# Optimization experiments

Hardware: AMD Instinct MI355X
Metric: run time of the kernel (lower is better)

Reference implementation:

```python
import jax, jax.numpy as jnp
import numpy as np

H_IMG, W_IMG = 16, 64
HK, WK = 7, 11
DIM, NUM_HEADS = 384, 8
BATCH = 32
SEQ = H_IMG * W_IMG  # 1024


def build_local_mask():
    # Faithful to the torch constructor: for each query position (i,j), a
    # (hk x wk) window of zeros in a padded canvas; everything else -inf.
    h, w, hk, wk = H_IMG, W_IMG, HK, WK
    mask = np.ones((h * w, h + hk - 1, w + wk - 1), dtype=np.float32)
    for i in range(h):
        for j in range(w):
            mask[w * i + j, i:i + hk, j:j + wk] = 0.0
    mask_c = mask[:, hk // 2:h + hk // 2, wk // 2:w + wk // 2].reshape(h * w, h * w)
    out = np.where(mask_c == 1.0, np.float32(-np.inf), mask_c).astype(np.float32)
    return jnp.asarray(out)  # [S, S]


def setup_inputs() -> dict:
    key = jax.random.key(0)
    k1, k2, k3, k4 = jax.random.split(key, 4)
    s = 1.0 / np.sqrt(DIM)
    return {
        "x": jax.random.normal(k1, (BATCH, SEQ, DIM), dtype=jnp.float32),
        "w_qkv": jax.random.normal(k2, (DIM, 3 * DIM), dtype=jnp.float32) * s,
        "w_proj": jax.random.normal(k3, (DIM, DIM), dtype=jnp.float32) * s,
        "b_proj": jax.random.normal(k4, (DIM,), dtype=jnp.float32) * 0.01,
        "mask": build_local_mask(),
    }


def reference(x, w_qkv, w_proj, b_proj, mask):
    B, S, C = x.shape
    H = NUM_HEADS
    D = C // H
    scale = D ** -0.5
    qkv = (x @ w_qkv).reshape(B, S, 3, H, D)
    qkv = jnp.transpose(qkv, (2, 0, 3, 1, 4))  # [3, B, H, S, D]
    q, k, v = qkv[0] * scale, qkv[1], qkv[2]
    attn = jnp.einsum("bhsd,bhtd->bhst", q, k)  # [B, H, S, S]
    attn = attn + mask[None, None]               # additive local-window bias
    attn = jax.nn.softmax(attn, axis=-1)
    out = jnp.einsum("bhst,bhtd->bhsd", attn, v)
    out = jnp.transpose(out, (0, 2, 1, 3)).reshape(B, S, C)
    return out @ w_proj + b_proj
```

## Files before the change

kernel.cpp:

```cpp
#include <hip/hip_runtime.h>
#include <hip/hip_bf16.h>


typedef __attribute__((ext_vector_type(8))) unsigned short ushort8;
typedef __attribute__((ext_vector_type(8))) short short8v;
typedef __attribute__((ext_vector_type(4))) float floatx4;

__device__ __forceinline__ float bf2f(unsigned short u) {
  union { unsigned int i; float f; } x;
  x.i = ((unsigned int)u) << 16;
  return x.f;
}

__device__ __forceinline__ unsigned short f2bu(float f) {
  union { float f; unsigned int i; } x;
  x.f = f;
  unsigned int lsb = (x.i >> 16) & 1u;
  x.i += 0x7FFFu + lsb;
  return (unsigned short)(x.i >> 16);
}

__device__ __forceinline__ unsigned int cvtpk_bf16(float lo, float hi) {
  unsigned int r;
  asm("v_cvt_pk_bf16_f32 %0, %1, %2" : "=v"(r) : "v"(lo), "v"(hi));
  return r;
}

__device__ __forceinline__ void gload_lds16(const void* g, void* l) {
  __builtin_amdgcn_global_load_lds(
      (const __attribute__((address_space(1))) unsigned int*)g,
      (__attribute__((address_space(3))) unsigned int*)l, 16, 0, 0);
}

__global__ __launch_bounds__(256) void transpose_cvt(
    const float* __restrict__ in, unsigned short* __restrict__ out, int R, int C) {
  __shared__ float t[32][33];
  const int c0 = blockIdx.x * 32, r0 = blockIdx.y * 32;
  const int tx = threadIdx.x, ty = threadIdx.y;
  #pragma unroll
  for (int rr = ty; rr < 32; rr += 8) t[rr][tx] = in[(size_t)(r0 + rr) * C + c0 + tx];
  __syncthreads();
  #pragma unroll
  for (int rr = ty; rr < 32; rr += 8)
    out[(size_t)(c0 + rr) * R + r0 + tx] = f2bu(t[tx][rr]);
}

__global__ __launch_bounds__(512) void gemm_qkv(
    const float* __restrict__ X,
    const unsigned short* __restrict__ Bt,
    unsigned short* __restrict__ qws, unsigned short* __restrict__ kws,
    unsigned short* __restrict__ vtws)
{
  __shared__ unsigned short smem[32768];
  const int tid = threadIdx.x;
  const int lane = tid & 63, w = tid >> 6;
  const int wm = w & 3, wn = w >> 2;

  const int nbx = gridDim.x;
  const int nwg = nbx * gridDim.y;
  const int bid = blockIdx.y * nbx + blockIdx.x;
  const int swz = (bid & 7) * (nwg >> 3) + (bid >> 3);
  const int n0 = (swz % nbx) * 128;
  const int m0 = (swz / nbx) * 128;

  floatx4 acc[2][4];
  #pragma unroll
  for (int mi = 0; mi < 2; ++mi)
    #pragma unroll
    for (int ni = 0; ni < 4; ++ni)
      acc[mi][ni] = (floatx4){0.f, 0.f, 0.f, 0.f};

  const int arow = tid >> 2;
  const int aslot = tid & 3;
  const int adst = arow * 64 + ((aslot * 16) ^ ((arow & 3) << 4));
  const float* asrc = X + (size_t)(m0 + arow) * 384 + aslot * 8;

  auto ASB = [&](int buf) -> char* { return (char*)smem + buf * 8192; };
  auto BSB = [&](int buf) -> char* { return (char*)smem + 32768 + buf * 8192; };

  float4 bank0[4], bank1[4];

  auto LOADA = [&](float4* bank, int p) {
    #pragma unroll
    for (int tile = 0; tile < 2; ++tile) {
      const float* s = asrc + (p * 2 + tile) * 32;
      bank[tile * 2 + 0] = *reinterpret_cast<const float4*>(s);
      bank[tile * 2 + 1] = *reinterpret_cast<const float4*>(s + 4);
    }
  };
  auto DSWRITE = [&](const float4* bank, int p) {
    #pragma unroll
    for (int tile = 0; tile < 2; ++tile) {
      const float4 f0 = bank[tile * 2 + 0];
      const float4 f1 = bank[tile * 2 + 1];
      uint4 v;
      v.x = cvtpk_bf16(f0.x, f0.y); v.y = cvtpk_bf16(f0.z, f0.w);
      v.z = cvtpk_bf16(f1.x, f1.y); v.w = cvtpk_bf16(f1.z, f1.w);
      *reinterpret_cast<uint4*>(ASB(2 * (p & 1) + tile) + adst) = v;
    }
  };
  const int srow = tid >> 2;
  const int kslot16 = (tid & 3) * 16;
  auto BGLOAD = [&](int p) {
    #pragma unroll
    for (int tile = 0; tile < 2; ++tile) {
      const int t = p * 2 + tile;
      const int kb = kslot16 ^ ((srow & 3) << 4);
      gload_lds16((const char*)Bt + (size_t)(n0 + srow) * 768 + t * 64 + kb,
                  BSB(2 * (p & 1) + tile) + w * 1024);
    }
  };
  auto COMPUTE = [&](int buf) {
    short8v a[2], b[4];
    const int kgb = (lane >> 4) * 16;
    #pragma unroll
    for (int mi = 0; mi < 2; ++mi) {
      const int r = wm * 32 + mi * 16 + (lane & 15);
      a[mi] = *reinterpret_cast<const short8v*>(
          ASB(buf) + r * 64 + (kgb ^ ((r & 3) << 4)));
    }
    #pragma unroll
    for (int ni = 0; ni < 4; ++ni) {
      const int r = wn * 64 + ni * 16 + (lane & 15);
      b[ni] = *reinterpret_cast<const short8v*>(
          BSB(buf) + r * 64 + (kgb ^ ((r & 3) << 4)));
    }
    #pragma unroll
    for (int mi = 0; mi < 2; ++mi)
      #pragma unroll
      for (int ni = 0; ni < 4; ++ni)
        acc[mi][ni] = __builtin_amdgcn_mfma_f32_16x16x32_bf16(
            a[mi], b[ni], acc[mi][ni], 0, 0, 0);
  };

  LOADA(bank0, 0);
  BGLOAD(0);
  LOADA(bank1, 1);
  BGLOAD(1);
  asm volatile("s_waitcnt vmcnt(8)" ::: "memory");
  DSWRITE(bank0, 0);
  asm volatile("s_waitcnt vmcnt(2)" ::: "memory");
  DSWRITE(bank1, 1);
  LOADA(bank0, 2);
  asm volatile("s_waitcnt lgkmcnt(0)" ::: "memory");
  __builtin_amdgcn_s_barrier();

  #pragma unroll
  for (int s = 0; s < 6; ++s) {
    __builtin_amdgcn_s_setprio(1);
    COMPUTE(2 * (s & 1));
    COMPUTE(2 * (s & 1) + 1);
    __builtin_amdgcn_s_setprio(0);
    asm volatile("s_waitcnt lgkmcnt(0)" ::: "memory");
    if (s + 2 <= 5) {
      asm volatile("s_waitcnt vmcnt(4)" ::: "memory");
    } else if (s + 1 <= 5) {
      asm volatile("s_waitcnt vmcnt(0)" ::: "memory");
    }
    __builtin_amdgcn_s_barrier();
    if (s + 2 <= 5) {
      BGLOAD(s + 2);
      asm volatile("s_waitcnt vmcnt(2)" ::: "memory");
      DSWRITE((s & 1) ? bank1 : bank0, s + 2);
      if (s + 3 <= 5) LOADA((s & 1) ? bank0 : bank1, s + 3);
    }
  }

  const int col_l = lane & 15;
  const int row_l = (lane >> 4) * 4;
  const float QSCALE = 0.14433756729740643f;
  const int which = n0 / 384;

  if (which < 2) {
    unsigned short* dstb = (which == 0) ? qws : kws;
    const float scale = (which == 0) ? QSCALE : 1.f;
    #pragma unroll
    for (int ni = 0; ni < 4; ++ni) {
      const int cg = n0 + wn * 64 + ni * 16 + col_l;
      const int rem = cg - which * 384;
      const int h = rem / 48;
      const int d = rem - h * 48;
      #pragma unroll
      for (int mi = 0; mi < 2; ++mi) {
        #pragma unroll
        for (int reg = 0; reg < 4; ++reg) {
          const int r = m0 + wm * 32 + mi * 16 + row_l + reg;
          const int bb = r >> 10, s = r & 1023;
          dstb[(((size_t)(bb * 8 + h)) * 1024 + s) * 48 + d] =
              f2bu(acc[mi][ni][reg] * scale);
        }
      }
    }
  } else {
    unsigned short* T = smem;
    #pragma unroll
    for (int ni = 0; ni < 4; ++ni) {
      const int col = wn * 64 + ni * 16 + col_l;
      #pragma unroll
      for (int mi = 0; mi < 2; ++mi) {
        const int rowb = wm * 32 + mi * 16 + row_l;
        #pragma unroll
        for (int reg = 0; reg < 4; ++reg)
          T[col * 136 + rowb + reg] = f2bu(acc[mi][ni][reg]);
      }
    }
    __syncthreads();
    const int col = tid >> 2, q = tid & 3;
    const int cg = n0 + col;
    const int rem = cg - 768;
    const int h = rem / 48, d = rem - h * 48;
    const int bb = m0 >> 10;
    const int s0 = (m0 & 1023) + q * 32;
    unsigned short* dst =
        vtws + (((size_t)(bb * 8 + h)) * 48 + d) * 1024 + s0;
    const unsigned short* src = T + col * 136 + q * 32;
    #pragma unroll
    for (int j = 0; j < 4; ++j)
      *reinterpret_cast<ushort8*>(dst + j * 8) =
          *reinterpret_cast<const ushort8*>(src + j * 8);
  }
}

__global__ __launch_bounds__(512) void gemm_proj(
    const unsigned short* __restrict__ A,
    const unsigned short* __restrict__ Bt,
    const float* __restrict__ bias, float* __restrict__ outf)
{
  __shared__ unsigned short smem[32768];
  const int tid = threadIdx.x;
  const int lane = tid & 63, w = tid >> 6;
  const int wm = w & 3, wn = w >> 2;

  const int nbx = gridDim.x;
  const int nwg = nbx * gridDim.y;
  const int bid = blockIdx.y * nbx + blockIdx.x;
  const int swz = (bid & 7) * (nwg >> 3) + (bid >> 3);
  const int n0 = (swz % nbx) * 128;
  const int m0 = (swz / nbx) * 128;

  floatx4 acc[2][4];
  #pragma unroll
  for (int mi = 0; mi < 2; ++mi)
    #pragma unroll
    for (int ni = 0; ni < 4; ++ni)
      acc[mi][ni] = (floatx4){0.f, 0.f, 0.f, 0.f};

  const int srow = tid >> 2;
  const int kslot16 = (tid & 3) * 16;

  auto ASB = [&](int buf) -> char* { return (char*)smem + buf * 8192; };
  auto BSB = [&](int buf) -> char* { return (char*)smem + 32768 + buf * 8192; };

  auto STAGE = [&](int buf, int k0) {
    const int kb = kslot16 ^ ((srow & 3) << 4);
    gload_lds16((const char*)A + (size_t)(m0 + srow) * 768 + k0 * 2 + kb,
                ASB(buf) + w * 1024);
    gload_lds16((const char*)Bt + (size_t)(n0 + srow) * 768 + k0 * 2 + kb,
                BSB(buf) + w * 1024);
  };

  auto COMPUTE = [&](int buf) {
    short8v a[2], b[4];
    const int kgb = (lane >> 4) * 16;
    #pragma unroll
    for (int mi = 0; mi < 2; ++mi) {
      const int r = wm * 32 + mi * 16 + (lane & 15);
      a[mi] = *reinterpret_cast<const short8v*>(
          ASB(buf) + r * 64 + (kgb ^ ((r & 3) << 4)));
    }
    #pragma unroll
    for (int ni = 0; ni < 4; ++ni) {
      const int r = wn * 64 + ni * 16 + (lane & 15);
      b[ni] = *reinterpret_cast<const short8v*>(
          BSB(buf) + r * 64 + (kgb ^ ((r & 3) << 4)));
    }
    #pragma unroll
    for (int mi = 0; mi < 2; ++mi)
      #pragma unroll
      for (int ni = 0; ni < 4; ++ni)
        acc[mi][ni] = __builtin_amdgcn_mfma_f32_16x16x32_bf16(
            a[mi], b[ni], acc[mi][ni], 0, 0, 0);
  };

  STAGE(0, 0);
  STAGE(1, 32);

  #pragma unroll
  for (int s = 0; s < 6; ++s) {
    const int rb = (s & 1) * 2;
    const int sb = rb ^ 2;
    if (s < 5) {
      STAGE(sb, (2 * s + 2) * 32);
      STAGE(sb + 1, (2 * s + 3) * 32);
      asm volatile("s_waitcnt vmcnt(4)" ::: "memory");
    } else {
      asm volatile("s_waitcnt vmcnt(0)" ::: "memory");
    }
    __builtin_amdgcn_s_barrier();
    __builtin_amdgcn_s_setprio(1);
    COMPUTE(rb);
    COMPUTE(rb + 1);
    __builtin_amdgcn_s_setprio(0);
    asm volatile("s_waitcnt lgkmcnt(0)" ::: "memory");
    __builtin_amdgcn_s_barrier();
  }

  const int col_l = lane & 15;
  const int row_l = (lane >> 4) * 4;
  #pragma unroll
  for (int ni = 0; ni < 4; ++ni) {
    const int cg = n0 + wn * 64 + ni * 16 + col_l;
    const float bv = bias[cg];
    #pragma unroll
    for (int mi = 0; mi < 2; ++mi) {
      #pragma unroll
      for (int reg = 0; reg < 4; ++reg) {
        const int r = m0 + wm * 32 + mi * 16 + row_l + reg;
        outf[(size_t)r * 384 + cg] = acc[mi][ni][reg] + bv;
      }
    }
  }
}

__global__ __launch_bounds__(256) void attn_mfma(
    const unsigned short* __restrict__ qws,
    const unsigned short* __restrict__ kws,
    const unsigned short* __restrict__ vt,
    unsigned short* __restrict__ attn_out)
{
  __shared__ unsigned short plds_all[4 * 64 * 72];

  const int tid = threadIdx.x;
  const int w = tid >> 6;
  const int lane = tid & 63;
  const int blk = blockIdx.x;
  const int sw = ((blk & 7) << 7) | (blk >> 3);
  const int task = sw * 4 + w;
  const int i  = task & 15;
  const int bh = task >> 4;
  const int ql = lane & 15;
  const int g  = lane >> 4;

  unsigned short* plds = plds_all + w * 4608;

  {
    const uint4 zz = make_uint4(0, 0, 0, 0);
    #pragma unroll
    for (int z = 0; z < 9; ++z)
      reinterpret_cast<uint4*>(plds)[lane + z * 64] = zz;
  }

  const unsigned short* qbase = qws + (size_t)bh * 1024 * 48;
  const unsigned short* kbase = kws + (size_t)bh * 1024 * 48;
  const unsigned short* vbase = vt  + (size_t)bh * 48 * 1024;

  const short8v zfrag = (short8v){0, 0, 0, 0, 0, 0, 0, 0};

  short8v qf[4][2];
  #pragma unroll
  for (int qt = 0; qt < 4; ++qt) {
    const unsigned short* qrow = qbase + (size_t)(i * 64 + qt * 16 + ql) * 48;
    qf[qt][0] = *reinterpret_cast<const short8v*>(qrow + 8 * g);
    qf[qt][1] = (g < 2) ? *reinterpret_cast<const short8v*>(qrow + 32 + 8 * g)
                        : zfrag;
  }

  floatx4 ot[3][4];
  #pragma unroll
  for (int dt = 0; dt < 3; ++dt)
    #pragma unroll
    for (int qt = 0; qt < 4; ++qt)
      ot[dt][qt] = (floatx4){0.f, 0.f, 0.f, 0.f};
  float mreg[4] = {-INFINITY, -INFINITY, -INFINITY, -INFINITY};
  float lreg[4] = {0.f, 0.f, 0.f, 0.f};

  const int ki0 = (i - 3 < 0) ? 0 : i - 3;
  const int ki1 = (i + 3 > 15) ? 15 : i + 3;

  for (int ki = ki0; ki <= ki1; ++ki) {
    short8v kf[4][2];
    #pragma unroll
    for (int kt = 0; kt < 4; ++kt) {
      const unsigned short* krow = kbase + (size_t)(ki * 64 + kt * 16 + ql) * 48;
      kf[kt][0] = *reinterpret_cast<const short8v*>(krow + 8 * g);
      kf[kt][1] = (g < 2) ? *reinterpret_cast<const short8v*>(krow + 32 + 8 * g)
                          : zfrag;
    }
    short8v vf[3][2];
    #pragma unroll
    for (int dt = 0; dt < 3; ++dt)
      #pragma unroll
      for (int c = 0; c < 2; ++c)
        vf[dt][c] = *reinterpret_cast<const short8v*>(
            vbase + (size_t)(16 * dt + ql) * 1024 + ki * 64 + 32 * c + 8 * g);

    #pragma unroll
    for (int qt = 0; qt < 4; ++qt) {
      const int kts = (qt == 0) ? 0 : qt - 1;
      const int kte = (qt == 3) ? 3 : qt + 1;
      floatx4 s[4];
      #pragma unroll
      for (int kt = 0; kt < 4; ++kt) {
        if (kt < kts || kt > kte) continue;
        s[kt] = __builtin_amdgcn_mfma_f32_16x16x32_bf16(
            kf[kt][0], qf[qt][0], (floatx4){0.f, 0.f, 0.f, 0.f}, 0, 0, 0);
        s[kt] = __builtin_amdgcn_mfma_f32_16x16x32_bf16(
            kf[kt][1], qf[qt][1], s[kt], 0, 0, 0);
      }
      const int qcol = qt * 16 + ql;
      float pmax = -INFINITY;
      #pragma unroll
      for (int kt = 0; kt < 4; ++kt) {
        if (kt < kts || kt > kte) continue;
        #pragma unroll
        for (int r = 0; r < 4; ++r) {
          const int delta = kt * 16 + 4 * g + r - qcol;
          const bool ok = (delta <= 5) && (delta >= -5);
          s[kt][r] = ok ? s[kt][r] : -INFINITY;
          pmax = fmaxf(pmax, s[kt][r]);
        }
      }
      if (!__all(pmax - mreg[qt] <= 8.0f)) {
        float mt = fmaxf(pmax, __shfl_xor(pmax, 16, 64));
        mt = fmaxf(mt, __shfl_xor(mt, 32, 64));
        const float mnew = fmaxf(mreg[qt], mt);
        const float corr = __expf(mreg[qt] - mnew);
        lreg[qt] *= corr;
        #pragma unroll
        for (int dt = 0; dt < 3; ++dt) {
          ot[dt][qt][0] *= corr; ot[dt][qt][1] *= corr;
          ot[dt][qt][2] *= corr; ot[dt][qt][3] *= corr;
        }
        mreg[qt] = mnew;
      }
      float ps = 0.f;
      #pragma unroll
      for (int kt = 0; kt < 4; ++kt) {
        if (kt < kts || kt > kte) continue;
        #pragma unroll
        for (int r = 0; r < 4; ++r) {
          const float p = __expf(s[kt][r] - mreg[qt]);
          s[kt][r] = p;
          ps += p;
        }
      }
      ps += __shfl_xor(ps, 16, 64);
      ps += __shfl_xor(ps, 32, 64);
      lreg[qt] += ps;
      #pragma unroll
      for (int kt = 0; kt < 4; ++kt) {
        if (kt < kts || kt > kte) continue;
        uint2 pk;
        pk.x = (unsigned int)f2bu(s[kt][0]) | ((unsigned int)f2bu(s[kt][1]) << 16);
        pk.y = (unsigned int)f2bu(s[kt][2]) | ((unsigned int)f2bu(s[kt][3]) << 16);
        *reinterpret_cast<uint2*>(&plds[(qt * 16 + ql) * 72 + kt * 16 + 4 * g]) = pk;
      }
    }

    __builtin_amdgcn_s_setprio(1);
    #pragma unroll
    for (int qt = 0; qt < 4; ++qt) {
      #pragma unroll
      for (int c = 0; c < 2; ++c) {
        if ((qt == 0 && c == 1) || (qt == 3 && c == 0)) continue;
        const short8v pf = *reinterpret_cast<const short8v*>(
            &plds[(qt * 16 + ql) * 72 + 32 * c + 8 * g]);
        #pragma unroll
        for (int dt = 0; dt < 3; ++dt)
          ot[dt][qt] = __builtin_amdgcn_mfma_f32_16x16x32_bf16(
              vf[dt][c], pf, ot[dt][qt], 0, 0, 0);
      }
    }
    __builtin_amdgcn_s_setprio(0);
  }

  const int b = bh >> 3, h = bh & 7;
  #pragma unroll
  for (int qt = 0; qt < 4; ++qt) {
    const float inv = 1.0f / lreg[qt];
    unsigned short* orow =
        attn_out + (size_t)(b * 1024 + i * 64 + qt * 16 + ql) * 384 + h * 48;
    #pragma unroll
    for (int dt = 0; dt < 3; ++dt) {
      const int d0 = 16 * dt + 4 * g;
      unsigned int w0 = (unsigned int)f2bu(ot[dt][qt][0] * inv) |
                        ((unsigned int)f2bu(ot[dt][qt][1] * inv) << 16);
      unsigned int w1 = (unsigned int)f2bu(ot[dt][qt][2] * inv) |
                        ((unsigned int)f2bu(ot[dt][qt][3] * inv) << 16);
      *reinterpret_cast<unsigned int*>(orow + d0)     = w0;
      *reinterpret_cast<unsigned int*>(orow + d0 + 2) = w1;
    }
  }
}

extern "C" void kernel_launch(void* const* d_in, const int* in_sizes, int n_in,
                              void* d_out, int out_size, void* d_ws, size_t ws_size,
                              hipStream_t stream) {
  const float* x      = (const float*)d_in[0];
  const float* w_qkv  = (const float*)d_in[1];
  const float* w_proj = (const float*)d_in[2];
  const float* b_proj = (const float*)d_in[3];

  const size_t T = 25165824;
  char* ws = (char*)d_ws;
  unsigned short* attn_out = (unsigned short*)ws;
  unsigned short* qws   = (unsigned short*)(ws + T);
  unsigned short* kws   = (unsigned short*)(ws + 2 * T);
  unsigned short* vtws  = (unsigned short*)(ws + 3 * T);
  unsigned short* wqkvT = (unsigned short*)(ws + 4 * T);
  unsigned short* wpT   = (unsigned short*)(ws + 4 * T + 884736);
  float* out = (float*)d_out;

  transpose_cvt<<<dim3(36, 12), dim3(32, 8), 0, stream>>>(w_qkv, wqkvT, 384, 1152);
  transpose_cvt<<<dim3(12, 12), dim3(32, 8), 0, stream>>>(w_proj, wpT, 384, 384);

  gemm_qkv<<<dim3(9, 256), 512, 0, stream>>>(x, wqkvT, qws, kws, vtws);
  attn_mfma<<<dim3(1024), 256, 0, stream>>>(qws, kws, vtws, attn_out);
  gemm_proj<<<dim3(3, 256), 512, 0, stream>>>(attn_out, wpT, b_proj, out);
}
```

Before: 131.0 us.

## Split each attention row-block task across two waves by query-tile halves

Each 64-query row block is now handled by two waves, each owning two of the four 16-query tiles and loading only the three key tiles it needs. The grid doubles to 2048 blocks, the per-wave LDS buffer halves, and registers per wave drop. This raises parallelism and occupancy for the attention kernel, at the cost of every key-block V tile being loaded by both waves and the per-block launch overhead doubling.

```diff
diff --git a/kernel.cpp b/kernel.cpp
--- a/kernel.cpp
+++ b/kernel.cpp
@@ -328,26 +328,30 @@
     const unsigned short* __restrict__ vt,
     unsigned short* __restrict__ attn_out)
 {
-  __shared__ unsigned short plds_all[4 * 64 * 72];
+  __shared__ unsigned short plds_all[4 * 32 * 72];
 
   const int tid = threadIdx.x;
   const int w = tid >> 6;
   const int lane = tid & 63;
   const int blk = blockIdx.x;
-  const int sw = ((blk & 7) << 7) | (blk >> 3);
-  const int task = sw * 4 + w;
+  const int sw = ((blk & 7) << 8) | (blk >> 3);
+  const int task = sw * 2 + (w >> 1);
+  const int half = w & 1;
   const int i  = task & 15;
   const int bh = task >> 4;
   const int ql = lane & 15;
   const int g  = lane >> 4;
-
-  unsigned short* plds = plds_all + w * 4608;
+  const int ktbase = half;
+
+  unsigned short* plds = plds_all + w * 2304;
 
   {
     const uint4 zz = make_uint4(0, 0, 0, 0);
     #pragma unroll
-    for (int z = 0; z < 9; ++z)
+    for (int z = 0; z < 4; ++z)
       reinterpret_cast<uint4*>(plds)[lane + z * 64] = zz;
+    if (lane < 32)
+      reinterpret_cast<uint4*>(plds)[lane + 256] = zz;
   }
 
   const unsigned short* qbase = qws + (size_t)bh * 1024 * 48;
@@ -356,35 +360,37 @@
 
   const short8v zfrag = (short8v){0, 0, 0, 0, 0, 0, 0, 0};
 
-  short8v qf[4][2];
-  #pragma unroll
-  for (int qt = 0; qt < 4; ++qt) {
+  short8v qf[2][2];
+  #pragma unroll
+  for (int lq = 0; lq < 2; ++lq) {
+    const int qt = half * 2 + lq;
     const unsigned short* qrow = qbase + (size_t)(i * 64 + qt * 16 + ql) * 48;
-    qf[qt][0] = *reinterpret_cast<const short8v*>(qrow + 8 * g);
-    qf[qt][1] = (g < 2) ? *reinterpret_cast<const short8v*>(qrow + 32 + 8 * g)
+    qf[lq][0] = *reinterpret_cast<const short8v*>(qrow + 8 * g);
+    qf[lq][1] = (g < 2) ? *reinterpret_cast<const short8v*>(qrow + 32 + 8 * g)
                         : zfrag;
   }
 
-  floatx4 ot[3][4];
+  floatx4 ot[3][2];
   #pragma unroll
   for (int dt = 0; dt < 3; ++dt)
     #pragma unroll
-    for (int qt = 0; qt < 4; ++qt)
-      ot[dt][qt] = (floatx4){0.f, 0.f, 0.f, 0.f};
-  float mreg[4] = {-INFINITY, -INFINITY, -INFINITY, -INFINITY};
-  float lreg[4] = {0.f, 0.f, 0.f, 0.f};
+    for (int lq = 0; lq < 2; ++lq)
+      ot[dt][lq] = (floatx4){0.f, 0.f, 0.f, 0.f};
+  float mreg[2] = {-INFINITY, -INFINITY};
+  float lreg[2] = {0.f, 0.f};
 
   const int ki0 = (i - 3 < 0) ? 0 : i - 3;
   const int ki1 = (i + 3 > 15) ? 15 : i + 3;
 
   for (int ki = ki0; ki <= ki1; ++ki) {
-    short8v kf[4][2];
-    #pragma unroll
-    for (int kt = 0; kt < 4; ++kt) {
+    short8v kf[3][2];
+    #pragma unroll
+    for (int j = 0; j < 3; ++j) {
+      const int kt = ktbase + j;
       const unsigned short* krow = kbase + (size_t)(ki * 64 + kt * 16 + ql) * 48;
-      kf[kt][0] = *reinterpret_cast<const short8v*>(krow + 8 * g);
-      kf[kt][1] = (g < 2) ? *reinterpret_cast<const short8v*>(krow + 32 + 8 * g)
-                          : zfrag;
+      kf[j][0] = *reinterpret_cast<const short8v*>(krow + 8 * g);
+      kf[j][1] = (g < 2) ? *reinterpret_cast<const short8v*>(krow + 32 + 8 * g)
+                         : zfrag;
     }
     short8v vf[3][2];
     #pragma unroll
@@ -395,80 +401,87 @@
             vbase + (size_t)(16 * dt + ql) * 1024 + ki * 64 + 32 * c + 8 * g);
 
     #pragma unroll
-    for (int qt = 0; qt < 4; ++qt) {
+    for (int lq = 0; lq < 2; ++lq) {
+      const int qt = half * 2 + lq;
       const int kts = (qt == 0) ? 0 : qt - 1;
       const int kte = (qt == 3) ? 3 : qt + 1;
-      floatx4 s[4];
-      #pragma unroll
-      for (int kt = 0; kt < 4; ++kt) {
+      floatx4 s[3];
+      #pragma unroll
+      for (int j = 0; j < 3; ++j) {
+        const int kt = ktbase + j;
         if (kt < kts || kt > kte) continue;
-        s[kt] = __builtin_amdgcn_mfma_f32_16x16x32_bf16(
-            kf[kt][0], qf[qt][0], (floatx4){0.f, 0.f, 0.f, 0.f}, 0, 0, 0);
-        s[kt] = __builtin_amdgcn_mfma_f32_16x16x32_bf16(
-            kf[kt][1], qf[qt][1], s[kt], 0, 0, 0);
+        s[j] = __builtin_amdgcn_mfma_f32_16x16x32_bf16(
+            kf[j][0], qf[lq][0], (floatx4){0.f, 0.f, 0.f, 0.f}, 0, 0, 0);
+        s[j] = __builtin_amdgcn_mfma_f32_16x16x32_bf16(
+            kf[j][1], qf[lq][1], s[j], 0, 0, 0);
       }
       const int qcol = qt * 16 + ql;
       float pmax = -INFINITY;
       #pragma unroll
-      for (int kt = 0; kt < 4; ++kt) {
+      for (int j = 0; j < 3; ++j) {
+        const int kt = ktbase + j;
         if (kt < kts || kt > kte) continue;
         #pragma unroll
         for (int r = 0; r < 4; ++r) {
           const int delta = kt * 16 + 4 * g + r - qcol;
           const bool ok = (delta <= 5) && (delta >= -5);
-          s[kt][r] = ok ? s[kt][r] : -INFINITY;
-          pmax = fmaxf(pmax, s[kt][r]);
+          s[j][r] = ok ? s[j][r] : -INFINITY;
+          pmax = fmaxf(pmax, s[j][r]);
         }
       }
-      if (!__all(pmax - mreg[qt] <= 8.0f)) {
+      if (!__all(pmax - mreg[lq] <= 8.0f)) {
         float mt = fmaxf(pmax, __shfl_xor(pmax, 16, 64));
         mt = fmaxf(mt, __shfl_xor(mt, 32, 64));
-        const float mnew = fmaxf(mreg[qt], mt);
-        const float corr = __expf(mreg[qt] - mnew);
-        lreg[qt] *= corr;
+        const float mnew = fmaxf(mreg[lq], mt);
+        const float corr = __expf(mreg[lq] - mnew);
+        lreg[lq] *= corr;
         #pragma unroll
         for (int dt = 0; dt < 3; ++dt) {
-          ot[dt][qt][0] *= corr; ot[dt][qt][1] *= corr;
-          ot[dt][qt][2] *= corr; ot[dt][qt][3] *= corr;
+          ot[dt][lq][0] *= corr; ot[dt][lq][1] *= corr;
+          ot[dt][lq][2] *= corr; ot[dt][lq][3] *= corr;
         }
-        mreg[qt] = mnew;
+        mreg[lq] = mnew;
       }
       float ps = 0.f;
       #pragma unroll
-      for (int kt = 0; kt < 4; ++kt) {
+      for (int j = 0; j < 3; ++j) {
+        const int kt = ktbase + j;
         if (kt < kts || kt > kte) continue;
         #pragma unroll
         for (int r = 0; r < 4; ++r) {
-          const float p = __expf(s[kt][r] - mreg[qt]);
-          s[kt][r] = p;
+          const float p = __expf(s[j][r] - mreg[lq]);
+          s[j][r] = p;
           ps += p;
         }
       }
       ps += __shfl_xor(ps, 16, 64);
       ps += __shfl_xor(ps, 32, 64);
-      lreg[qt] += ps;
-      #pragma unroll
-      for (int kt = 0; kt < 4; ++kt) {
+      lreg[lq] += ps;
+      #pragma unroll
+      for (int j = 0; j < 3; ++j) {
+        const int kt = ktbase + j;
         if (kt < kts || kt > kte) continue;
         uint2 pk;
-        pk.x = (unsigned int)f2bu(s[kt][0]) | ((unsigned int)f2bu(s[kt][1]) << 16);
-        pk.y = (unsigned int)f2bu(s[kt][2]) | ((unsigned int)f2bu(s[kt][3]) << 16);
-        *reinterpret_cast<uint2*>(&plds[(qt * 16 + ql) * 72 + kt * 16 + 4 * g]) = pk;
+        pk.x = (unsigned int)f2bu(s[j][0]) | ((unsigned int)f2bu(s[j][1]) << 16);
+        pk.y = (unsigned int)f2bu(s[j][2]) | ((unsigned int)f2bu(s[j][3]) << 16);
+        *reinterpret_cast<uint2*>(
+            &plds[(lq * 16 + ql) * 72 + kt * 16 + 4 * g]) = pk;
       }
     }
 
     __builtin_amdgcn_s_setprio(1);
     #pragma unroll
-    for (int qt = 0; qt < 4; ++qt) {
+    for (int lq = 0; lq < 2; ++lq) {
+      const int qt = half * 2 + lq;
       #pragma unroll
       for (int c = 0; c < 2; ++c) {
         if ((qt == 0 && c == 1) || (qt == 3 && c == 0)) continue;
         const short8v pf = *reinterpret_cast<const short8v*>(
-            &plds[(qt * 16 + ql) * 72 + 32 * c + 8 * g]);
+            &plds[(lq * 16 + ql) * 72 + 32 * c + 8 * g]);
         #pragma unroll
         for (int dt = 0; dt < 3; ++dt)
-          ot[dt][qt] = __builtin_amdgcn_mfma_f32_16x16x32_bf16(
-              vf[dt][c], pf, ot[dt][qt], 0, 0, 0);
+          ot[dt][lq] = __builtin_amdgcn_mfma_f32_16x16x32_bf16(
+              vf[dt][c], pf, ot[dt][lq], 0, 0, 0);
       }
     }
     __builtin_amdgcn_s_setprio(0);
@@ -476,17 +489,18 @@
 
   const int b = bh >> 3, h = bh & 7;
   #pragma unroll
-  for (int qt = 0; qt < 4; ++qt) {
-    const float inv = 1.0f / lreg[qt];
+  for (int lq = 0; lq < 2; ++lq) {
+    const int qt = half * 2 + lq;
+    const float inv = 1.0f / lreg[lq];
     unsigned short* orow =
         attn_out + (size_t)(b * 1024 + i * 64 + qt * 16 + ql) * 384 + h * 48;
     #pragma unroll
     for (int dt = 0; dt < 3; ++dt) {
       const int d0 = 16 * dt + 4 * g;
-      unsigned int w0 = (unsigned int)f2bu(ot[dt][qt][0] * inv) |
-                        ((unsigned int)f2bu(ot[dt][qt][1] * inv) << 16);
-      unsigned int w1 = (unsigned int)f2bu(ot[dt][qt][2] * inv) |
-                        ((unsigned int)f2bu(ot[dt][qt][3] * inv) << 16);
+      unsigned int w0 = (unsigned int)f2bu(ot[dt][lq][0] * inv) |
+                        ((unsigned int)f2bu(ot[dt][lq][1] * inv) << 16);
+      unsigned int w1 = (unsigned int)f2bu(ot[dt][lq][2] * inv) |
+                        ((unsigned int)f2bu(ot[dt][lq][3] * inv) << 16);
       *reinterpret_cast<unsigned int*>(orow + d0)     = w0;
       *reinterpret_cast<unsigned int*>(orow + d0 + 2) = w1;
     }
@@ -515,6 +529,6 @@
   transpose_cvt<<<dim3(12, 12), dim3(32, 8), 0, stream>>>(w_proj, wpT, 384, 384);
 
   gemm_qkv<<<dim3(9, 256), 512, 0, stream>>>(x, wqkvT, qws, kws, vtws);
-  attn_mfma<<<dim3(1024), 256, 0, stream>>>(qws, kws, vtws, attn_out);
+  attn_mfma<<<dim3(2048), 256, 0, stream>>>(qws, kws, vtws, attn_out);
   gemm_proj<<<dim3(3, 256), 512, 0, stream>>>(attn_out, wpT, b_proj, out);
 }
```

After: 141.4 us. +7.9%, slower.
